# Kernel tuning notes

Measured on AMD Instinct MI355X. Metric: run time of the kernel, lower is better.

Reference implementation:

```python
import jax, jax.numpy as jnp
import numpy as np

B, H, S, DK = 1, 16, 4096, 64
SQRT_DK = float(DK) ** 0.5


def setup_inputs() -> dict:
    key = jax.random.key(0)
    kq, kk, kv = jax.random.split(key, 3)
    q = jax.random.normal(kq, (B, H, S, DK), dtype=jnp.float32)
    k = jax.random.normal(kk, (B, H, S, DK), dtype=jnp.float32)
    v = jax.random.normal(kv, (B, H, S, DK), dtype=jnp.float32)
    # causal mask: 1 where attention allowed, 0 where masked
    mask = jnp.tril(jnp.ones((S, S), dtype=jnp.int32))[None, None, :, :]
    return {"q": q, "k": k, "v": v, "mask": mask}


def reference(q, k, v, mask):
    # score = q @ k^T / sqrt(d_k)  -> [B, H, S, S]
    score = jnp.einsum("bhqd,bhkd->bhqk", q, k) / SQRT_DK
    # masked_fill(mask == 0, -inf)
    score = jnp.where(mask == 0, -jnp.inf, score)
    attn = jax.nn.softmax(score, axis=-1)
    # dropout with p=0.0 is identity
    return jnp.einsum("bhqk,bhkd->bhqd", attn, v)
```

## Files before the change

### kernel.cpp

```cpp
#include <hip/hip_runtime.h>

#define NH 16
#define SEQ 4096
#define DK 64
#define LSTR 72

typedef __fp16   fp16x2 __attribute__((ext_vector_type(2)));
typedef _Float16 f16x2 __attribute__((ext_vector_type(2)));
typedef _Float16 f16x4 __attribute__((ext_vector_type(4)));
typedef _Float16 f16x8 __attribute__((ext_vector_type(8)));
typedef float    f32x4 __attribute__((ext_vector_type(4)));

__device__ __forceinline__ f16x4 pk4(float a, float b, float c, float d) {
    f16x2 lo = __builtin_bit_cast(f16x2, (fp16x2)__builtin_amdgcn_cvt_pkrtz(a, b));
    f16x2 hi = __builtin_bit_cast(f16x2, (fp16x2)__builtin_amdgcn_cvt_pkrtz(c, d));
    f16x4 r; r[0] = lo[0]; r[1] = lo[1]; r[2] = hi[0]; r[3] = hi[1];
    return r;
}
__device__ __forceinline__ f16x4 lo4(f16x8 x) {
    return __builtin_shufflevector(x, x, 0, 1, 2, 3);
}
__device__ __forceinline__ f16x4 hi4(f16x8 x) {
    return __builtin_shufflevector(x, x, 4, 5, 6, 7);
}


__global__ __launch_bounds__(512, 4) void sdpa_flash_v3(
    const float* __restrict__ q, const float* __restrict__ k,
    const float* __restrict__ v, float* __restrict__ out)
{
    __shared__ _Float16 Ks[64 * LSTR];
    __shared__ _Float16 Vt[64 * LSTR];

    const int t    = threadIdx.x;
    const int wave = t >> 6;
    const int lane = t & 63;
    const int ln   = lane & 15;
    const int quad = lane >> 4;

    const int h    = blockIdx.x & (NH - 1);
    const int pair = blockIdx.x >> 4;
    const int qA0  = pair * 64;
    const int qB0  = (63 - pair) * 64;
    const int qw   = ((wave < 4) ? qA0 : qB0) + (wave & 3) * 16;

    const float SC = 0.125f * 1.44269504088896f;

    const float* qp = q + ((size_t)h * SEQ + qw + ln) * DK + quad * 4;
    f16x4 qf[4];
#pragma unroll
    for (int kf = 0; kf < 4; ++kf) {
        float4 x = *(const float4*)(qp + kf * 16);
        qf[kf] = pk4(x.x, x.y, x.z, x.w);
    }

    f32x4 O[4];
#pragma unroll
    for (int i = 0; i < 4; ++i) O[i] = (f32x4){0.f, 0.f, 0.f, 0.f};
    float l = 0.f;

    const float4* kh4 = (const float4*)(k + (size_t)h * SEQ * DK);
    const float*  vhp = v + (size_t)h * SEQ * DK;
    const int vd = t & 63, vw = t >> 6;

    for (int k0 = 0; k0 <= qB0; k0 += 64) {
        __syncthreads();
#pragma unroll
        for (int i = 0; i < 2; ++i) {
            const int idx = i * 512 + t;
            const int key = idx >> 4, c4 = idx & 15;
            float4 kk = kh4[k0 * 16 + idx];
            const int c = (c4 & 3) * 16 + (c4 >> 2) * 4;
            *(f16x4*)&Ks[key * LSTR + c] = pk4(kk.x, kk.y, kk.z, kk.w);
        }
#pragma unroll
        for (int i = 0; i < 2; ++i) {
            const int m = i * 8 + vw;
            const float* vp = vhp + (size_t)(k0 + 4 * m) * DK + vd;
            float x0 = vp[0], x1 = vp[DK], x2 = vp[2 * DK], x3 = vp[3 * DK];
            const int c = (m & 3) * 16 + (m >> 2) * 4;
            *(f16x4*)&Vt[vd * LSTR + c] = pk4(x0, x1, x2, x3);
        }
        __syncthreads();

        if (k0 > qw + 15) continue;
        const bool diag = (k0 + 63 > qw);

        f16x4 pf[4];
        float lt = 0.f;
#pragma unroll
        for (int ksub = 0; ksub < 4; ++ksub) {
            const _Float16* kr = &Ks[(ksub * 16 + ln) * LSTR + quad * 16];
            f16x8 a01 = *(const f16x8*)kr;
            f16x8 a23 = *(const f16x8*)(kr + 8);
            f32x4 acc = (f32x4){0.f, 0.f, 0.f, 0.f};
            acc = __builtin_amdgcn_mfma_f32_16x16x16f16(lo4(a01), qf[0], acc, 0, 0, 0);
            acc = __builtin_amdgcn_mfma_f32_16x16x16f16(hi4(a01), qf[1], acc, 0, 0, 0);
            acc = __builtin_amdgcn_mfma_f32_16x16x16f16(lo4(a23), qf[2], acc, 0, 0, 0);
            acc = __builtin_amdgcn_mfma_f32_16x16x16f16(hi4(a23), qf[3], acc, 0, 0, 0);
            if (diag) {
                const int keyb = k0 + ksub * 16 + quad * 4;
#pragma unroll
                for (int r = 0; r < 4; ++r)
                    if (keyb + r > qw + ln) acc[r] = -1e30f;
            }
            float p0 = __builtin_amdgcn_exp2f(fmaf(acc[0], SC, -12.f));
            float p1 = __builtin_amdgcn_exp2f(fmaf(acc[1], SC, -12.f));
            float p2 = __builtin_amdgcn_exp2f(fmaf(acc[2], SC, -12.f));
            float p3 = __builtin_amdgcn_exp2f(fmaf(acc[3], SC, -12.f));
            lt += (p0 + p1) + (p2 + p3);
            pf[ksub] = pk4(p0, p1, p2, p3);
        }
        l += lt;

#pragma unroll
        for (int dsub = 0; dsub < 4; ++dsub) {
            const _Float16* vr = &Vt[(dsub * 16 + ln) * LSTR + quad * 16];
            f16x8 v01 = *(const f16x8*)vr;
            f16x8 v23 = *(const f16x8*)(vr + 8);
            O[dsub] = __builtin_amdgcn_mfma_f32_16x16x16f16(lo4(v01), pf[0], O[dsub], 0, 0, 0);
            O[dsub] = __builtin_amdgcn_mfma_f32_16x16x16f16(hi4(v01), pf[1], O[dsub], 0, 0, 0);
            O[dsub] = __builtin_amdgcn_mfma_f32_16x16x16f16(lo4(v23), pf[2], O[dsub], 0, 0, 0);
            O[dsub] = __builtin_amdgcn_mfma_f32_16x16x16f16(hi4(v23), pf[3], O[dsub], 0, 0, 0);
        }
    }

    l += __shfl_xor(l, 16);
    l += __shfl_xor(l, 32);
    const float inv = 1.f / l;

    float* op = out + ((size_t)h * SEQ + qw + ln) * DK + quad * 4;
#pragma unroll
    for (int dsub = 0; dsub < 4; ++dsub) {
        float4 r;
        r.x = O[dsub][0] * inv; r.y = O[dsub][1] * inv;
        r.z = O[dsub][2] * inv; r.w = O[dsub][3] * inv;
        *(float4*)(op + dsub * 16) = r;
    }
}

extern "C" void kernel_launch(void* const* d_in, const int* in_sizes, int n_in,
                              void* d_out, int out_size, void* d_ws, size_t ws_size,
                              hipStream_t stream) {
    const float* q = (const float*)d_in[0];
    const float* k = (const float*)d_in[1];
    const float* v = (const float*)d_in[2];
    float* out = (float*)d_out;

    dim3 grid(NH * 32);
    dim3 block(512);
    sdpa_flash_v3<<<grid, block, 0, stream>>>(q, k, v, out);
}
```

Before: 222.1 us.

## Double-buffer K/V tiles with register prefetch and 32-row queries per wave

Each wave now handles two 16-row query groups, sharing every K/V fragment read from LDS across both, and the block shrinks to 256 threads. K and V tiles go into double-buffered LDS in a pre-swizzled, fragment-ordered layout, and the next tile is prefetched into registers while the current one is computed. This drops one barrier per iteration and hides global load latency. The cost is more registers per thread and possibly lower occupancy.

```diff
diff --git a/kernel.cpp b/kernel.cpp
--- a/kernel.cpp
+++ b/kernel.cpp
@@ -3,7 +3,6 @@
 #define NH 16
 #define SEQ 4096
 #define DK 64
-#define LSTR 72
 
 typedef __fp16   fp16x2 __attribute__((ext_vector_type(2)));
 typedef _Float16 f16x2 __attribute__((ext_vector_type(2)));
@@ -14,23 +13,18 @@
 __device__ __forceinline__ f16x4 pk4(float a, float b, float c, float d) {
     f16x2 lo = __builtin_bit_cast(f16x2, (fp16x2)__builtin_amdgcn_cvt_pkrtz(a, b));
     f16x2 hi = __builtin_bit_cast(f16x2, (fp16x2)__builtin_amdgcn_cvt_pkrtz(c, d));
-    f16x4 r; r[0] = lo[0]; r[1] = lo[1]; r[2] = hi[0]; r[3] = hi[1];
+    f16x4 r; r[0]=lo[0]; r[1]=lo[1]; r[2]=hi[0]; r[3]=hi[1];
     return r;
 }
-__device__ __forceinline__ f16x4 lo4(f16x8 x) {
-    return __builtin_shufflevector(x, x, 0, 1, 2, 3);
-}
-__device__ __forceinline__ f16x4 hi4(f16x8 x) {
-    return __builtin_shufflevector(x, x, 4, 5, 6, 7);
-}
+__device__ __forceinline__ f16x4 lo4(f16x8 x){return __builtin_shufflevector(x,x,0,1,2,3);}
+__device__ __forceinline__ f16x4 hi4(f16x8 x){return __builtin_shufflevector(x,x,4,5,6,7);}
 
-
-__global__ __launch_bounds__(512, 4) void sdpa_flash_v3(
+__global__ __launch_bounds__(256) void sdpa_flash_v5(
     const float* __restrict__ q, const float* __restrict__ k,
     const float* __restrict__ v, float* __restrict__ out)
 {
-    __shared__ _Float16 Ks[64 * LSTR];
-    __shared__ _Float16 Vt[64 * LSTR];
+    __shared__ _Float16 Ks[2][4096];
+    __shared__ _Float16 Vt[2][4096];
 
     const int t    = threadIdx.x;
     const int wave = t >> 6;
@@ -42,100 +36,137 @@
     const int pair = blockIdx.x >> 4;
     const int qA0  = pair * 64;
     const int qB0  = (63 - pair) * 64;
-    const int qw   = ((wave < 4) ? qA0 : qB0) + (wave & 3) * 16;
+    const int qw   = ((wave < 2) ? qA0 : qB0) + (wave & 1) * 32;
 
     const float SC = 0.125f * 1.44269504088896f;
 
-    const float* qp = q + ((size_t)h * SEQ + qw + ln) * DK + quad * 4;
-    f16x4 qf[4];
+    f16x4 qf[2][4];
 #pragma unroll
-    for (int kf = 0; kf < 4; ++kf) {
-        float4 x = *(const float4*)(qp + kf * 16);
-        qf[kf] = pk4(x.x, x.y, x.z, x.w);
+    for (int g = 0; g < 2; ++g) {
+        const float* qp = q + ((size_t)h * SEQ + qw + g * 16 + ln) * DK + quad * 4;
+#pragma unroll
+        for (int kf = 0; kf < 4; ++kf) {
+            float4 x = *(const float4*)(qp + kf * 16);
+            qf[g][kf] = pk4(x.x, x.y, x.z, x.w);
+        }
     }
 
-    f32x4 O[4];
+    f32x4 O[2][4];
 #pragma unroll
-    for (int i = 0; i < 4; ++i) O[i] = (f32x4){0.f, 0.f, 0.f, 0.f};
-    float l = 0.f;
+    for (int g = 0; g < 2; ++g)
+#pragma unroll
+        for (int i = 0; i < 4; ++i) O[g][i] = (f32x4){0.f, 0.f, 0.f, 0.f};
+    float l[2] = {0.f, 0.f};
 
     const float4* kh4 = (const float4*)(k + (size_t)h * SEQ * DK);
     const float*  vhp = v + (size_t)h * SEQ * DK;
-    const int vd = t & 63, vw = t >> 6;
 
+    int koff[4], lin4[4];
+    const float* vp0[4];
+#pragma unroll
+    for (int i = 0; i < 4; ++i) {
+        const int linear = i * 256 + t;
+        const int blk8   = linear >> 7;
+        const int within = linear & 127;
+        const int ln_ = within >> 3;
+        const int qd_ = (within >> 1) & 3;
+        const int u_  = within & 1;
+        const int sub = blk8 >> 1, b = blk8 & 1;
+        const int g_  = 2 * b + u_;
+        koff[i] = (sub * 16 + ln_) * 16 + (g_ * 4 + qd_);
+        vp0[i]  = vhp + (size_t)(g_ * 16 + qd_ * 4) * DK + sub * 16 + ln_;
+        lin4[i] = linear * 4;
+    }
+
+    float4 kpre[4];
+    float  vpre[4][4];
+#pragma unroll
+    for (int i = 0; i < 4; ++i) {
+        kpre[i] = kh4[koff[i]];
+        const float* p = vp0[i];
+#pragma unroll
+        for (int j = 0; j < 4; ++j) vpre[i][j] = p[j * DK];
+    }
+
+    int buf = 0;
     for (int k0 = 0; k0 <= qB0; k0 += 64) {
-        __syncthreads();
 #pragma unroll
-        for (int i = 0; i < 2; ++i) {
-            const int idx = i * 512 + t;
-            const int key = idx >> 4, c4 = idx & 15;
-            float4 kk = kh4[k0 * 16 + idx];
-            const int c = (c4 & 3) * 16 + (c4 >> 2) * 4;
-            *(f16x4*)&Ks[key * LSTR + c] = pk4(kk.x, kk.y, kk.z, kk.w);
-        }
-#pragma unroll
-        for (int i = 0; i < 2; ++i) {
-            const int m = i * 8 + vw;
-            const float* vp = vhp + (size_t)(k0 + 4 * m) * DK + vd;
-            float x0 = vp[0], x1 = vp[DK], x2 = vp[2 * DK], x3 = vp[3 * DK];
-            const int c = (m & 3) * 16 + (m >> 2) * 4;
-            *(f16x4*)&Vt[vd * LSTR + c] = pk4(x0, x1, x2, x3);
+        for (int i = 0; i < 4; ++i) {
+            *(f16x4*)&Ks[buf][lin4[i]] = pk4(kpre[i].x, kpre[i].y, kpre[i].z, kpre[i].w);
+            *(f16x4*)&Vt[buf][lin4[i]] = pk4(vpre[i][0], vpre[i][1], vpre[i][2], vpre[i][3]);
         }
         __syncthreads();
-
-        if (k0 > qw + 15) continue;
-        const bool diag = (k0 + 63 > qw);
-
-        f16x4 pf[4];
-        float lt = 0.f;
+        if (k0 < qB0) {
+            const int kn = k0 + 64;
 #pragma unroll
-        for (int ksub = 0; ksub < 4; ++ksub) {
-            const _Float16* kr = &Ks[(ksub * 16 + ln) * LSTR + quad * 16];
-            f16x8 a01 = *(const f16x8*)kr;
-            f16x8 a23 = *(const f16x8*)(kr + 8);
-            f32x4 acc = (f32x4){0.f, 0.f, 0.f, 0.f};
-            acc = __builtin_amdgcn_mfma_f32_16x16x16f16(lo4(a01), qf[0], acc, 0, 0, 0);
-            acc = __builtin_amdgcn_mfma_f32_16x16x16f16(hi4(a01), qf[1], acc, 0, 0, 0);
-            acc = __builtin_amdgcn_mfma_f32_16x16x16f16(lo4(a23), qf[2], acc, 0, 0, 0);
-            acc = __builtin_amdgcn_mfma_f32_16x16x16f16(hi4(a23), qf[3], acc, 0, 0, 0);
-            if (diag) {
-                const int keyb = k0 + ksub * 16 + quad * 4;
+            for (int i = 0; i < 4; ++i) {
+                kpre[i] = kh4[kn * 16 + koff[i]];
+                const float* p = vp0[i] + (size_t)kn * DK;
 #pragma unroll
-                for (int r = 0; r < 4; ++r)
-                    if (keyb + r > qw + ln) acc[r] = -1e30f;
+                for (int j = 0; j < 4; ++j) vpre[i][j] = p[j * DK];
             }
-            float p0 = __builtin_amdgcn_exp2f(fmaf(acc[0], SC, -12.f));
-            float p1 = __builtin_amdgcn_exp2f(fmaf(acc[1], SC, -12.f));
-            float p2 = __builtin_amdgcn_exp2f(fmaf(acc[2], SC, -12.f));
-            float p3 = __builtin_amdgcn_exp2f(fmaf(acc[3], SC, -12.f));
-            lt += (p0 + p1) + (p2 + p3);
-            pf[ksub] = pk4(p0, p1, p2, p3);
         }
-        l += lt;
+        if (k0 <= qw + 31) {
+            const bool diag = (k0 + 63 > qw);
+            f16x4 pf[2][4];
+#pragma unroll
+            for (int ksub = 0; ksub < 4; ++ksub) {
+                const _Float16* kr = &Ks[buf][(ksub * 2) * 512 + ln * 32 + quad * 8];
+                f16x8 a01 = *(const f16x8*)kr;
+                f16x8 a23 = *(const f16x8*)(kr + 512);
+#pragma unroll
+                for (int g = 0; g < 2; ++g) {
+                    f32x4 acc = (f32x4){0.f, 0.f, 0.f, 0.f};
+                    acc = __builtin_amdgcn_mfma_f32_16x16x16f16(lo4(a01), qf[g][0], acc, 0, 0, 0);
+                    acc = __builtin_amdgcn_mfma_f32_16x16x16f16(hi4(a01), qf[g][1], acc, 0, 0, 0);
+                    acc = __builtin_amdgcn_mfma_f32_16x16x16f16(lo4(a23), qf[g][2], acc, 0, 0, 0);
+                    acc = __builtin_amdgcn_mfma_f32_16x16x16f16(hi4(a23), qf[g][3], acc, 0, 0, 0);
+                    if (diag) {
+                        const int keyb = k0 + ksub * 16 + quad * 4;
+                        const int qrow = qw + g * 16 + ln;
+#pragma unroll
+                        for (int r = 0; r < 4; ++r)
+                            if (keyb + r > qrow) acc[r] = -1e30f;
+                    }
+                    float p0 = __builtin_amdgcn_exp2f(fmaf(acc[0], SC, -12.f));
+                    float p1 = __builtin_amdgcn_exp2f(fmaf(acc[1], SC, -12.f));
+                    float p2 = __builtin_amdgcn_exp2f(fmaf(acc[2], SC, -12.f));
+                    float p3 = __builtin_amdgcn_exp2f(fmaf(acc[3], SC, -12.f));
+                    l[g] += (p0 + p1) + (p2 + p3);
+                    pf[g][ksub] = pk4(p0, p1, p2, p3);
+                }
+            }
+#pragma unroll
+            for (int dsub = 0; dsub < 4; ++dsub) {
+                const _Float16* vr = &Vt[buf][(dsub * 2) * 512 + ln * 32 + quad * 8];
+                f16x8 v01 = *(const f16x8*)vr;
+                f16x8 v23 = *(const f16x8*)(vr + 512);
+#pragma unroll
+                for (int g = 0; g < 2; ++g) {
+                    O[g][dsub] = __builtin_amdgcn_mfma_f32_16x16x16f16(lo4(v01), pf[g][0], O[g][dsub], 0, 0, 0);
+                    O[g][dsub] = __builtin_amdgcn_mfma_f32_16x16x16f16(hi4(v01), pf[g][1], O[g][dsub], 0, 0, 0);
+                    O[g][dsub] = __builtin_amdgcn_mfma_f32_16x16x16f16(lo4(v23), pf[g][2], O[g][dsub], 0, 0, 0);
+                    O[g][dsub] = __builtin_amdgcn_mfma_f32_16x16x16f16(hi4(v23), pf[g][3], O[g][dsub], 0, 0, 0);
+                }
+            }
+        }
+        buf ^= 1;
+    }
 
 #pragma unroll
+    for (int g = 0; g < 2; ++g) {
+        float lg = l[g];
+        lg += __shfl_xor(lg, 16);
+        lg += __shfl_xor(lg, 32);
+        const float inv = 1.f / lg;
+        float* op = out + ((size_t)h * SEQ + qw + g * 16 + ln) * DK + quad * 4;
+#pragma unroll
         for (int dsub = 0; dsub < 4; ++dsub) {
-            const _Float16* vr = &Vt[(dsub * 16 + ln) * LSTR + quad * 16];
-            f16x8 v01 = *(const f16x8*)vr;
-            f16x8 v23 = *(const f16x8*)(vr + 8);
-            O[dsub] = __builtin_amdgcn_mfma_f32_16x16x16f16(lo4(v01), pf[0], O[dsub], 0, 0, 0);
-            O[dsub] = __builtin_amdgcn_mfma_f32_16x16x16f16(hi4(v01), pf[1], O[dsub], 0, 0, 0);
-            O[dsub] = __builtin_amdgcn_mfma_f32_16x16x16f16(lo4(v23), pf[2], O[dsub], 0, 0, 0);
-            O[dsub] = __builtin_amdgcn_mfma_f32_16x16x16f16(hi4(v23), pf[3], O[dsub], 0, 0, 0);
+            float4 r;
+            r.x = O[g][dsub][0] * inv; r.y = O[g][dsub][1] * inv;
+            r.z = O[g][dsub][2] * inv; r.w = O[g][dsub][3] * inv;
+            *(float4*)(op + dsub * 16) = r;
         }
-    }
-
-    l += __shfl_xor(l, 16);
-    l += __shfl_xor(l, 32);
-    const float inv = 1.f / l;
-
-    float* op = out + ((size_t)h * SEQ + qw + ln) * DK + quad * 4;
-#pragma unroll
-    for (int dsub = 0; dsub < 4; ++dsub) {
-        float4 r;
-        r.x = O[dsub][0] * inv; r.y = O[dsub][1] * inv;
-        r.z = O[dsub][2] * inv; r.w = O[dsub][3] * inv;
-        *(float4*)(op + dsub * 16) = r;
     }
 }
 
@@ -148,6 +179,6 @@
     float* out = (float*)d_out;
 
     dim3 grid(NH * 32);
-    dim3 block(512);
-    sdpa_flash_v3<<<grid, block, 0, stream>>>(q, k, v, out);
+    dim3 block(256);
+    sdpa_flash_v5<<<grid, block, 0, stream>>>(q, k, v, out);
 }
```

New measurement: 252.6 us. 13.7% more time.
